# Kernel optimization log

Measured on AMD Instinct MI355X. Metric: run time of the kernel, lower is better.

## Reference

```python
import jax, jax.numpy as jnp
import numpy as np

NHEADS = 16

def setup_inputs() -> dict:
    key = jax.random.key(0)
    ks = jax.random.split(key, 5)
    C = 1024
    d = C // NHEADS
    x  = jax.random.normal(ks[0], (2, 2048, C), dtype=jnp.float32)
    sc = 1.0 / np.sqrt(C)
    wq = jax.random.normal(ks[1], (C, C), dtype=jnp.float32) * sc
    wk = jax.random.normal(ks[2], (C, C), dtype=jnp.float32) * sc
    wv = jax.random.normal(ks[3], (C, C), dtype=jnp.float32) * sc
    wo = jax.random.normal(ks[4], (d, C), dtype=jnp.float32) * (1.0 / np.sqrt(d))
    return {"x": x, "wq": wq, "wk": wk, "wv": wv, "wo": wo}

def reference(x, wq, wk, wv, wo):
    B, T, C = x.shape
    H = NHEADS
    d = C // H

    def split_heads(y):
        return y.reshape(B, T, H, d).transpose(0, 2, 1, 3)  # [B,H,T,d]

    Q = split_heads(x @ wq)
    K = split_heads(x @ wk)
    V = split_heads(x @ wv)

    # scores[b,h,q,k]
    prod = jnp.einsum('bhqd,bhkd->bhqk', Q, K) / np.sqrt(d)

    # ALiBi bias: offset[h, q, k] = (k - q) * 2**(-8*(h+1)/H)
    idx = jnp.arange(T)
    slopes = jnp.exp2(-8.0 * (jnp.arange(H, dtype=jnp.float32) + 1.0) / H)
    bias = (idx[None, :] - idx[:, None]).astype(x.dtype) * slopes[:, None, None]
    prod = prod + bias[None]

    # causal tril mask: keep k <= q
    keep = idx[None, :] <= idx[:, None]  # [T_q, T_k]
    prod = jnp.where(keep[None, None], prod, -jnp.inf)

    # NOTE: original uses F.softmax(prod, 2) -> softmax over the QUERY axis.
    attention_weights = jax.nn.softmax(prod, axis=2)
    attention_output = jnp.einsum('bhqk,bhkd->bhqd', attention_weights, V)

    # per-head wo projection then sum over heads == (sum over heads) @ wo (linear)
    outputs = attention_output.sum(axis=1) @ wo  # [B,T,C]
    return x + outputs
```

## Files before the change

kernel.cpp:

```cpp
#include <hip/hip_runtime.h>
#include <math.h>

#define NB 2
#define NH 16
#define NT 2048
#define ND 64
#define NC 1024
#define L2E 1.44269504f

typedef __attribute__((ext_vector_type(4))) float f32x4;
typedef __attribute__((ext_vector_type(8))) short short8;
typedef __attribute__((ext_vector_type(4))) short short4_t;
typedef __attribute__((ext_vector_type(8))) unsigned short ushort8;
typedef __attribute__((ext_vector_type(4))) unsigned short ushort4_t;

#define GLOAD_LDS(gp, lp)                                                \
    __builtin_amdgcn_global_load_lds(                                    \
        (const __attribute__((address_space(1))) void*)(gp),             \
        (__attribute__((address_space(3))) void*)(lp), 16, 0, 0)

__device__ __forceinline__ int sigma_p(int p) {
    return 4 * ((p >> 3) & 3) + (p & 3) + 16 * ((p >> 2) & 1) + 32 * (p >> 5);
}

__device__ __forceinline__ unsigned short f2bf(float f) {
    unsigned u = __builtin_bit_cast(unsigned, f);
    unsigned r = (u + 0x7FFFu + ((u >> 16) & 1u)) >> 16;
    return (unsigned short)r;
}

__device__ __forceinline__ unsigned cvtpk_bf16(float lo, float hi) {
    unsigned r;
    asm("v_cvt_pk_bf16_f32 %0, %1, %2" : "=v"(r) : "v"(lo), "v"(hi));
    return r;
}

__device__ __forceinline__ f32x4 mfma16(short8 a, short8 b, f32x4 c) {
    return __builtin_amdgcn_mfma_f32_16x16x32_bf16(a, b, c, 0, 0, 0);
}

__device__ __forceinline__ short8 frag_load(const unsigned short* rowp, int g, int half) {
    short8 v;
    short4_t lo = *(const short4_t*)(rowp + 4 * g + 32 * half);
    short4_t hi = *(const short4_t*)(rowp + 4 * g + 16 + 32 * half);
    #pragma unroll
    for (int j = 0; j < 4; ++j) { v[j] = lo[j]; v[4 + j] = hi[j]; }
    return v;
}

__device__ __forceinline__ short8 frag_g(const unsigned short* rowp, int g, int half) {
    return *(const short8*)(rowp + 8 * g + 32 * half);
}

__device__ __forceinline__ short8 frag_swz128(const unsigned short* tile, int row, int g, int half) {
    const char* p = (const char*)tile + row * 128 + (((g + 4 * half) ^ (row & 7)) << 4);
    return *(const short8*)p;
}

__global__ __launch_bounds__(256) void cvt_x(const float* __restrict__ src,
                                             unsigned short* __restrict__ dst, int n4) {
    int i = blockIdx.x * 256 + threadIdx.x;
    if (i >= n4) return;
    const int blk = i >> 4, c4 = i & 15;
    const int gg = (c4 >> 1) & 3, bb = c4 & 1, hh = c4 >> 3;
    f32x4 v = ((const f32x4*)src)[blk * 16 + gg + 4 * bb + 8 * hh];
    ushort4_t o;
    #pragma unroll
    for (int j = 0; j < 4; ++j) o[j] = f2bf(v[j]);
    ((ushort4_t*)dst)[i] = o;
}

__global__ __launch_bounds__(256) void cvtT3(const float* __restrict__ w0,
                                             const float* __restrict__ w1,
                                             const float* __restrict__ w2,
                                             unsigned short* __restrict__ Wt_all) {
    __shared__ __align__(16) float T[64][68];
    const float* W = (blockIdx.z == 0) ? w0 : ((blockIdx.z == 1) ? w1 : w2);
    unsigned short* Wt = Wt_all + (size_t)blockIdx.z * NC * NC;
    const int tid = threadIdx.x;
    const int k0 = blockIdx.x * 64, n0 = blockIdx.y * 64;
    #pragma unroll
    for (int p = 0; p < 4; ++p) {
        int r = 16 * p + (tid >> 4);
        int c = (tid & 15) * 4;
        *(f32x4*)&T[r][c] = *(const f32x4*)&W[(size_t)(k0 + r) * NC + n0 + c];
    }
    __syncthreads();
    const int nr = tid >> 2, kc = (tid & 3) * 16;
    ushort8 o0, o1;
    #pragma unroll
    for (int j = 0; j < 8; ++j) o0[j] = f2bf(T[sigma_p(kc + j)][nr]);
    #pragma unroll
    for (int j = 0; j < 8; ++j) o1[j] = f2bf(T[sigma_p(kc + 8 + j)][nr]);
    unsigned short* q = Wt + (size_t)(n0 + nr) * NC + k0 + kc;
    *(ushort8*)q       = o0;
    *(ushort8*)(q + 8) = o1;
}

__global__ __launch_bounds__(256) void cvtT_wo(const float* __restrict__ W,
                                               unsigned short* __restrict__ Wt) {
    __shared__ __align__(16) float T[64][68];
    const int tid = threadIdx.x;
    const int n0 = blockIdx.y * 64;
    #pragma unroll
    for (int p = 0; p < 4; ++p) {
        int r = 16 * p + (tid >> 4);
        int c = (tid & 15) * 4;
        *(f32x4*)&T[r][c] = *(const f32x4*)&W[(size_t)r * NC + n0 + c];
    }
    __syncthreads();
    const int nr = tid >> 2, kc = (tid & 3) * 16;
    ushort8 o0, o1;
    #pragma unroll
    for (int j = 0; j < 8; ++j) { o0[j] = f2bf(T[kc + j][nr]); o1[j] = f2bf(T[kc + 8 + j][nr]); }
    unsigned short* q = Wt + (size_t)(n0 + nr) * ND + kc;
    *(ushort8*)q       = o0;
    *(ushort8*)(q + 8) = o1;
}

__global__ __launch_bounds__(256) void gemm_qkv(const unsigned short* __restrict__ Xh,
                                                const unsigned short* __restrict__ Wt_all,
                                                unsigned short* __restrict__ qk_dst,
                                                unsigned short* __restrict__ Vt) {
    __shared__ __align__(16) unsigned short Xs[2][8192];
    __shared__ __align__(16) unsigned short Ws[2][8192];
    const int tid = threadIdx.x;
    const int lane = tid & 63, w = tid >> 6;
    const int g = lane >> 4, l15 = lane & 15;
    const int wr = w >> 1, wc = w & 1;
    const int subrow = lane >> 3;
    const int src_off = (((lane & 7) ^ subrow) << 4);
    const int m0 = blockIdx.x * 128;
    const int which = blockIdx.y >> 3;
    const int n0 = (blockIdx.y & 7) * 128;
    const unsigned short* Wt = Wt_all + (size_t)which * NC * NC;

    f32x4 acc[4][4] = {};

    auto stage = [&](int buf, int kk) {
        #pragma unroll
        for (int i = 0; i < 4; ++i) {
            const int r0 = 8 * w + 32 * i;
            const char* xs = (const char*)Xh + (((size_t)(m0 + r0 + subrow) * NC + kk) << 1) + src_off;
            GLOAD_LDS(xs, (char*)&Xs[buf][r0 * 64]);
            const char* ws = (const char*)Wt + (((size_t)(n0 + r0 + subrow) * NC + kk) << 1) + src_off;
            GLOAD_LDS(ws, (char*)&Ws[buf][r0 * 64]);
        }
    };

    stage(0, 0);
    asm volatile("s_waitcnt vmcnt(0)" ::: "memory");
    __builtin_amdgcn_s_barrier();
    int cur = 0;

    for (int kk = 0; kk < NC; kk += 64) {
        if (kk + 64 < NC) stage(cur ^ 1, kk + 64);
        short8 a[4][2], b[4][2];
        #pragma unroll
        for (int mr = 0; mr < 4; ++mr) {
            a[mr][0] = frag_swz128(Xs[cur], 64 * wr + 16 * mr + l15, g, 0);
            a[mr][1] = frag_swz128(Xs[cur], 64 * wr + 16 * mr + l15, g, 1);
        }
        #pragma unroll
        for (int nc = 0; nc < 4; ++nc) {
            b[nc][0] = frag_swz128(Ws[cur], 64 * wc + 16 * nc + l15, g, 0);
            b[nc][1] = frag_swz128(Ws[cur], 64 * wc + 16 * nc + l15, g, 1);
        }
        #pragma unroll
        for (int mr = 0; mr < 4; ++mr)
            #pragma unroll
            for (int nc = 0; nc < 4; ++nc) {
                acc[mr][nc] = mfma16(a[mr][0], b[nc][0], acc[mr][nc]);
                acc[mr][nc] = mfma16(a[mr][1], b[nc][1], acc[mr][nc]);
            }
        asm volatile("s_waitcnt vmcnt(0)" ::: "memory");
        __builtin_amdgcn_s_barrier();
        cur ^= 1;
    }

    if (which < 2) {
        unsigned short* dst = qk_dst + (size_t)which * (NB * NH * NT * ND);
        #pragma unroll
        for (int mr = 0; mr < 4; ++mr) {
            #pragma unroll
            for (int nc = 0; nc < 4; ++nc) {
                const int n = n0 + 64 * wc + 16 * nc + l15;
                const int hh = n >> 6;
                const int dd = 32 * (nc >> 1) + 8 * (l15 >> 2) + 4 * (nc & 1) + (l15 & 3);
                #pragma unroll
                for (int r = 0; r < 4; ++r) {
                    const int m = m0 + 64 * wr + 16 * mr + 4 * g + r;
                    const int bb = m >> 11, tt = m & (NT - 1);
                    dst[(((size_t)bb * NH + hh) * NT + tt) * ND + dd] = f2bf(acc[mr][nc][r]);
                }
            }
        }
    } else {
        #pragma unroll
        for (int mr = 0; mr < 4; ++mr) {
            const int m = m0 + 64 * wr + 16 * mr + 4 * g;
            const int bb = m >> 11, tt = m & (NT - 1);
            const int tbase = (tt & ~63) + 32 * (mr >> 1) + 8 * g + 4 * (mr & 1);
            #pragma unroll
            for (int nc = 0; nc < 4; ++nc) {
                const int n = n0 + 64 * wc + 16 * nc + l15;
                const int hh = n >> 6, dd = n & 63;
                ushort4_t o;
                #pragma unroll
                for (int r = 0; r < 4; ++r) o[r] = f2bf(acc[mr][nc][r]);
                *(ushort4_t*)&Vt[(((size_t)bb * NH + hh) * ND + dd) * NT + tbase] = o;
            }
        }
    }
}

__global__ __launch_bounds__(256, 4) void colstats(const unsigned short* __restrict__ Qh,
                                                   const unsigned short* __restrict__ Kh,
                                                   float* __restrict__ Lc2) {
    __shared__ __align__(16) unsigned short Qs[3][4096];
    const int tid = threadIdx.x;
    const int lane = tid & 63, w = tid >> 6;
    const int g = lane >> 4, l15 = lane & 15;
    const int subrow = lane >> 3;
    const int src_off = (((lane & 7) ^ subrow) << 4);
    const int lin = blockIdx.x + 32 * blockIdx.y;
    const int xcd = lin & 7, idx = lin >> 3;
    const int bh = xcd * 4 + (idx & 3);
    const int rest = idx >> 2;
    const int j = rest >> 1, par = rest & 1;
    const int jA = j, jB = 31 - j;
    const int hh = bh & (NH - 1);
    const float slL2 = exp2f(-0.5f * (float)(hh + 1)) * L2E;
    const float C1 = 0.125f * L2E;
    const float s16 = 16.f * slL2;

    const int K0A = 64 * jA, K0B = 64 * jB;
    const unsigned short* krA = Kh + ((size_t)bh * NT + K0A + 16 * w + l15) * ND;
    const unsigned short* krB = Kh + ((size_t)bh * NT + K0B + 16 * w + l15) * ND;
    const short8 akA0 = frag_g(krA, g, 0), akA1 = frag_g(krA, g, 1);
    const short8 akB0 = frag_g(krB, g, 0), akB1 = frag_g(krB, g, 1);
    const int kA0 = K0A + 16 * w + 4 * g;
    const int kB0 = K0B + 16 * w + 4 * g;

    const char* Qbase = (const char*)(Qh + (size_t)bh * NT * ND);
    auto stage = [&](int buf, int q0) {
        const char* qs = Qbase + (size_t)(q0 + 16 * w + subrow) * 128 + src_off;
        char* qd = (char*)&Qs[buf][16 * w * 64];
        GLOAD_LDS(qs, qd);
        GLOAD_LDS(qs + 1024, qd + 1024);
    };

    f32x4 accA = {}, accB = {};
    float rs[4];
    #pragma unroll
    for (int r = 0; r < 4; ++r) rs[r] = (float)r * slL2;

    const int qt0 = jA + ((par ^ jA) & 1);
    stage(0, 64 * qt0);
    stage(1, 64 * (qt0 + 2));
    int cur = 0, nxt = 2;

    auto strip = [&](const short8* qf, const short8& a0, const short8& a1,
                     f32x4& acc, float b0, bool mask) {
        #pragma unroll
        for (int q4 = 0; q4 < 4; ++q4) {
            f32x4 d = {};
            __builtin_amdgcn_s_setprio(1);
            d = mfma16(a0, qf[2 * q4], d);
            d = mfma16(a1, qf[2 * q4 + 1], d);
            __builtin_amdgcn_s_setprio(0);
            #pragma unroll
            for (int r = 0; r < 4; ++r) {
                float e = exp2f(fmaf(d[r], C1, b0 + rs[r]));
                if (mask && (16 * q4 + l15 < 16 * w + 4 * g + r)) e = 0.f;
                acc[r] += e;
            }
            b0 -= s16;
        }
    };

    for (int qt = qt0; qt < 32; qt += 2) {
        if (qt + 2 < 32) asm volatile("s_waitcnt vmcnt(2)" ::: "memory");
        else             asm volatile("s_waitcnt vmcnt(0)" ::: "memory");
        __builtin_amdgcn_s_barrier();
        if (qt + 4 < 32) stage(nxt, 64 * (qt + 4));
        const unsigned short* tile = Qs[cur];
        short8 qf[8];
        #pragma unroll
        for (int q4 = 0; q4 < 4; ++q4) {
            qf[2 * q4]     = frag_swz128(tile, 16 * q4 + l15, g, 0);
            qf[2 * q4 + 1] = frag_swz128(tile, 16 * q4 + l15, g, 1);
        }
        const int q0 = 64 * qt;
        strip(qf, akA0, akA1, accA, (float)(kA0 - q0 - l15) * slL2, qt == jA);
        if (qt >= jB)
            strip(qf, akB0, akB1, accB, (float)(kB0 - q0 - l15) * slL2, qt == jB);
        cur = (cur == 2) ? 0 : cur + 1;
        nxt = (nxt == 2) ? 0 : nxt + 1;
    }
    #pragma unroll
    for (int off = 1; off <= 8; off <<= 1) {
        #pragma unroll
        for (int r = 0; r < 4; ++r) {
            accA[r] += __shfl_xor(accA[r], off);
            accB[r] += __shfl_xor(accB[r], off);
        }
    }
    if (l15 == 0) {
        float* Lp = Lc2 + (size_t)(par * 32 + bh) * NT;
        #pragma unroll
        for (int r = 0; r < 4; ++r) {
            Lp[kA0 + r] = accA[r];
            Lp[kB0 + r] = accB[r];
        }
    }
}

__global__ __launch_bounds__(256) void attn_pv(const unsigned short* __restrict__ Qh,
                                               const unsigned short* __restrict__ Kh,
                                               const unsigned short* __restrict__ Vt,
                                               const float* __restrict__ Lc2,
                                               float* __restrict__ att) {
    __shared__ __align__(16) unsigned short Ks[3][4096];
    __shared__ __align__(16) unsigned short Vs[3][4096];
    __shared__ __align__(16) float Ls[NT];
    const int tid = threadIdx.x;
    const int lane = tid & 63, w = tid >> 6;
    const int g = lane >> 4, l15 = lane & 15;
    const int subrow = lane >> 3;
    const int src_off = (((lane & 7) ^ subrow) << 4);
    const int lin = blockIdx.x + 16 * blockIdx.y;
    const int xcd = lin & 7, idx = lin >> 3;
    const int bh = xcd * 4 + (idx & 3);
    const int j = idx >> 2;
    const int jA = j, jB = 31 - j;
    const int Q0A = 64 * jA, Q0B = 64 * jB;
    const int qA = Q0A + 16 * w + l15;
    const int qB = Q0B + 16 * w + l15;
    const int hh = bh & (NH - 1);
    const int bb = bh >> 4;
    const float slL2 = exp2f(-0.5f * (float)(hh + 1)) * L2E;
    const float C1 = 0.125f * L2E;

    short8 bqA0, bqA1, bqB0, bqB1;
    {
        const unsigned short* qr = Qh + ((size_t)bh * NT + qA) * ND;
        bqA0 = frag_g(qr, g, 0);
        bqA1 = frag_g(qr, g, 1);
        qr = Qh + ((size_t)bh * NT + qB) * ND;
        bqB0 = frag_g(qr, g, 0);
        bqB1 = frag_g(qr, g, 1);
    }

    auto stageKV = [&](int buf, int K0) {
        const char* ksrc = (const char*)Kh + (size_t)((size_t)bh * NT + K0 + 16 * w + subrow) * 128 + src_off;
        char* kdst = (char*)&Ks[buf][16 * w * 64];
        GLOAD_LDS(ksrc, kdst);
        GLOAD_LDS(ksrc + 1024, kdst + 1024);
        const char* vsrc = (const char*)Vt + ((((size_t)bh * ND + 16 * w + subrow) * NT + K0) << 1) + src_off;
        char* vdst = (char*)&Vs[buf][16 * w * 64];
        GLOAD_LDS(vsrc, vdst);
        GLOAD_LDS(vsrc + 8 * NT * 2, vdst + 1024);
    };

    stageKV(0, 0);
    stageKV(1, 64);
    {
        const f32x4* La = (const f32x4*)(Lc2 + (size_t)bh * NT);
        const f32x4* Lb = (const f32x4*)(Lc2 + (size_t)(32 + bh) * NT);
        const int nv = (jB + 1) * 16;
        for (int i = tid; i < nv; i += 256) {
            f32x4 a = La[i], b = Lb[i];
            float kb = (float)(4 * i);
            f32x4 v;
            #pragma unroll
            for (int c = 0; c < 4; ++c)
                v[c] = log2f(a[c] + b[c]) - (kb + (float)c) * slL2;
            ((f32x4*)Ls)[i] = v;
        }
    }
    asm volatile("s_waitcnt lgkmcnt(0)" ::: "memory");
    int cur = 0, nxt = 2;

    f32x4 oA[4] = {}, oB[4] = {};
    const float qsA = (float)qA * slL2;
    const float qsB = (float)qB * slL2;

    auto dostrip = [&](const short8* kf, const short8* vf,
                       const short8& q0f, const short8& q1f, f32x4 (&o)[4],
                       float qsc, int q, int K0, bool mask) {
        f32x4 pacc[4];
        __builtin_amdgcn_s_setprio(1);
        #pragma unroll
        for (int s4 = 0; s4 < 4; ++s4) {
            f32x4 d = {};
            d = mfma16(kf[2 * s4], q0f, d);
            d = mfma16(kf[2 * s4 + 1], q1f, d);
            pacc[s4] = d;
        }
        __builtin_amdgcn_s_setprio(0);
        union { unsigned u[4]; short8 s; } pa[2];
        #pragma unroll
        for (int s4 = 0; s4 < 4; ++s4) {
            f32x4 Lf = *(const f32x4*)&Ls[K0 + 16 * s4 + 4 * g];
            float p[4];
            #pragma unroll
            for (int r = 0; r < 4; ++r)
                p[r] = exp2f(fmaf(pacc[s4][r], C1, -(Lf[r] + qsc)));
            if (mask) {
                #pragma unroll
                for (int r = 0; r < 4; ++r)
                    if (K0 + 16 * s4 + 4 * g + r > q) p[r] = 0.f;
            }
            pa[s4 >> 1].u[2 * (s4 & 1)]     = cvtpk_bf16(p[0], p[1]);
            pa[s4 >> 1].u[2 * (s4 & 1) + 1] = cvtpk_bf16(p[2], p[3]);
        }
        __builtin_amdgcn_s_setprio(1);
        #pragma unroll
        for (int n = 0; n < 4; ++n) {
            o[n] = mfma16(pa[0].s, vf[2 * n], o[n]);
            o[n] = mfma16(pa[1].s, vf[2 * n + 1], o[n]);
        }
        __builtin_amdgcn_s_setprio(0);
    };

    for (int kt = 0; kt <= jB; ++kt) {
        if (kt < jB) asm volatile("s_waitcnt vmcnt(4)" ::: "memory");
        else         asm volatile("s_waitcnt vmcnt(0)" ::: "memory");
        __builtin_amdgcn_s_barrier();
        if (kt + 2 <= jB) stageKV(nxt, 64 * (kt + 2));
        const int K0 = 64 * kt;
        short8 kf[8], vf[8];
        #pragma unroll
        for (int s4 = 0; s4 < 4; ++s4) {
            kf[2 * s4]     = frag_swz128(Ks[cur], 16 * s4 + l15, g, 0);
            kf[2 * s4 + 1] = frag_swz128(Ks[cur], 16 * s4 + l15, g, 1);
            vf[2 * s4]     = frag_swz128(Vs[cur], 16 * s4 + l15, g, 0);
            vf[2 * s4 + 1] = frag_swz128(Vs[cur], 16 * s4 + l15, g, 1);
        }
        dostrip(kf, vf, bqB0, bqB1, oB, qsB, qB, K0, kt == jB);
        if (kt <= jA)
            dostrip(kf, vf, bqA0, bqA1, oA, qsA, qA, K0, kt == jA);
        cur = (cur == 2) ? 0 : cur + 1;
        nxt = (nxt == 2) ? 0 : nxt + 1;
    }
    #pragma unroll
    for (int n = 0; n < 4; ++n) {
        #pragma unroll
        for (int r = 0; r < 4; ++r) {
            att[(((size_t)bb * NT + Q0A + 16 * w + 4 * g + r) * NH + hh) * ND + 16 * n + l15] = oA[n][r];
            att[(((size_t)bb * NT + Q0B + 16 * w + 4 * g + r) * NH + hh) * ND + 16 * n + l15] = oB[n][r];
        }
    }
}

__global__ __launch_bounds__(256) void headsum(const float* __restrict__ att,
                                               unsigned short* __restrict__ A) {
    const int row = blockIdx.x * 16 + (threadIdx.x >> 4);
    const int d0 = (threadIdx.x & 15) * 4;
    const float* p = att + (size_t)row * (NH * ND) + d0;
    f32x4 s = {};
    #pragma unroll
    for (int h = 0; h < NH; ++h)
        s += *(const f32x4*)(p + h * ND);
    ushort4_t o;
    #pragma unroll
    for (int j = 0; j < 4; ++j) o[j] = f2bf(s[j]);
    *(ushort4_t*)&A[(size_t)row * ND + d0] = o;
}

__global__ __launch_bounds__(256) void out_proj(const float* __restrict__ x,
                                                const unsigned short* __restrict__ A,
                                                const unsigned short* __restrict__ Wot,
                                                float* __restrict__ out) {
    const int tid = threadIdx.x;
    const int lane = tid & 63, w = tid >> 6;
    const int g = lane >> 4, l15 = lane & 15;
    const int m0 = blockIdx.x * 64, n0 = blockIdx.y * 64;

    const unsigned short* ar = A + (size_t)(m0 + 16 * w + l15) * ND;
    short8 a0 = frag_load(ar, g, 0);
    short8 a1 = frag_load(ar, g, 1);

    f32x4 acc[4] = {};
    #pragma unroll
    for (int ns = 0; ns < 4; ++ns) {
        const unsigned short* br = Wot + (size_t)(n0 + 16 * ns + l15) * ND;
        acc[ns] = mfma16(a0, frag_load(br, g, 0), acc[ns]);
        acc[ns] = mfma16(a1, frag_load(br, g, 1), acc[ns]);
    }
    #pragma unroll
    for (int ns = 0; ns < 4; ++ns) {
        #pragma unroll
        for (int r = 0; r < 4; ++r) {
            int m = m0 + 16 * w + 4 * g + r;
            int n = n0 + 16 * ns + l15;
            out[(size_t)m * NC + n] = x[(size_t)m * NC + n] + acc[ns][r];
        }
    }
}

extern "C" void kernel_launch(void* const* d_in, const int* in_sizes, int n_in,
                              void* d_out, int out_size, void* d_ws, size_t ws_size,
                              hipStream_t stream) {
    const float* x  = (const float*)d_in[0];
    const float* wq = (const float*)d_in[1];
    const float* wk = (const float*)d_in[2];
    const float* wv = (const float*)d_in[3];
    const float* wo = (const float*)d_in[4];
    float* out = (float*)d_out;

    const size_t MB = 1u << 20;
    const size_t KB = 1u << 10;
    unsigned char* w8 = (unsigned char*)d_ws;
    unsigned short* Xh  = (unsigned short*)(w8);
    unsigned short* Wta = (unsigned short*)(w8 + 8 * MB);
    unsigned short* Qh  = (unsigned short*)(w8 + 16 * MB);
    unsigned short* Kh  = (unsigned short*)(w8 + 24 * MB);
    unsigned short* Vt  = (unsigned short*)(w8 + 32 * MB);
    float*          att = (float*)(w8 + 40 * MB);
    float*          Lc2 = (float*)(w8 + 56 * MB);
    unsigned short* A   = (unsigned short*)(w8 + 56 * MB + 512 * KB);
    unsigned short* Wot = (unsigned short*)(w8 + 57 * MB);

    cvt_x<<<(NB * NT * NC) / 1024, 256, 0, stream>>>(x, Xh, (NB * NT * NC) / 4);
    cvtT3<<<dim3(16, 16, 3), 256, 0, stream>>>(wq, wk, wv, Wta);
    cvtT_wo<<<dim3(1, 16), 256, 0, stream>>>(wo, Wot);

    gemm_qkv<<<dim3(32, 24), 256, 0, stream>>>(Xh, Wta, Qh, Vt);

    colstats<<<dim3(32, 32), 256, 0, stream>>>(Qh, Kh, Lc2);
    attn_pv<<<dim3(16, 32), 256, 0, stream>>>(Qh, Kh, Vt, Lc2, att);

    headsum<<<(NB * NT) / 16, 256, 0, stream>>>(att, A);
    out_proj<<<dim3(64, 16), 256, 0, stream>>>(x, A, Wot, out);
}
```

Baseline: 142.7 us.

## Split attn_pv query strips across 8 waves instead of 4

The attn_pv kernel now launches 512 threads per block. Waves 0-3 handle the late (B) query strip and waves 4-7 the early (A) strip, where before each wave processed both strips one after the other. K/V staging is spread over 8 waves with one load each, and the vmcnt waits are adjusted to match. This doubles the number of waves that can hide latency and halves each wave's serial work. In exchange, the A-strip waves sit idle after their causal range ends but must still reach every barrier, and the higher thread count per block may limit occupancy through register pressure.

Result: no change. 141.1 us (-1.1%).

```diff
diff --git a/kernel.cpp b/kernel.cpp
--- a/kernel.cpp
+++ b/kernel.cpp
@@ -316,7 +316,7 @@
     }
 }
 
-__global__ __launch_bounds__(256) void attn_pv(const unsigned short* __restrict__ Qh,
+__global__ __launch_bounds__(512) void attn_pv(const unsigned short* __restrict__ Qh,
                                                const unsigned short* __restrict__ Kh,
                                                const unsigned short* __restrict__ Vt,
                                                const float* __restrict__ Lc2,
@@ -334,33 +334,29 @@
     const int bh = xcd * 4 + (idx & 3);
     const int j = idx >> 2;
     const int jA = j, jB = 31 - j;
-    const int Q0A = 64 * jA, Q0B = 64 * jB;
-    const int qA = Q0A + 16 * w + l15;
-    const int qB = Q0B + 16 * w + l15;
     const int hh = bh & (NH - 1);
     const int bb = bh >> 4;
     const float slL2 = exp2f(-0.5f * (float)(hh + 1)) * L2E;
     const float C1 = 0.125f * L2E;
 
-    short8 bqA0, bqA1, bqB0, bqB1;
+    const bool isB = (w < 4);
+    const int wl = isB ? w : (w - 4);
+    const int Q0 = isB ? 64 * jB : 64 * jA;
+    const int myJ = isB ? jB : jA;
+    const int q = Q0 + 16 * wl + l15;
+
+    short8 bq0, bq1;
     {
-        const unsigned short* qr = Qh + ((size_t)bh * NT + qA) * ND;
-        bqA0 = frag_g(qr, g, 0);
-        bqA1 = frag_g(qr, g, 1);
-        qr = Qh + ((size_t)bh * NT + qB) * ND;
-        bqB0 = frag_g(qr, g, 0);
-        bqB1 = frag_g(qr, g, 1);
+        const unsigned short* qr = Qh + ((size_t)bh * NT + q) * ND;
+        bq0 = frag_g(qr, g, 0);
+        bq1 = frag_g(qr, g, 1);
     }
 
     auto stageKV = [&](int buf, int K0) {
-        const char* ksrc = (const char*)Kh + (size_t)((size_t)bh * NT + K0 + 16 * w + subrow) * 128 + src_off;
-        char* kdst = (char*)&Ks[buf][16 * w * 64];
-        GLOAD_LDS(ksrc, kdst);
-        GLOAD_LDS(ksrc + 1024, kdst + 1024);
-        const char* vsrc = (const char*)Vt + ((((size_t)bh * ND + 16 * w + subrow) * NT + K0) << 1) + src_off;
-        char* vdst = (char*)&Vs[buf][16 * w * 64];
-        GLOAD_LDS(vsrc, vdst);
-        GLOAD_LDS(vsrc + 8 * NT * 2, vdst + 1024);
+        const char* ksrc = (const char*)Kh + (size_t)((size_t)bh * NT + K0 + 8 * w + subrow) * 128 + src_off;
+        GLOAD_LDS(ksrc, (char*)&Ks[buf][8 * w * 64]);
+        const char* vsrc = (const char*)Vt + ((((size_t)bh * ND + 8 * w + subrow) * NT + K0) << 1) + src_off;
+        GLOAD_LDS(vsrc, (char*)&Vs[buf][8 * w * 64]);
     };
 
     stageKV(0, 0);
@@ -369,7 +365,7 @@
         const f32x4* La = (const f32x4*)(Lc2 + (size_t)bh * NT);
         const f32x4* Lb = (const f32x4*)(Lc2 + (size_t)(32 + bh) * NT);
         const int nv = (jB + 1) * 16;
-        for (int i = tid; i < nv; i += 256) {
+        for (int i = tid; i < nv; i += 512) {
             f32x4 a = La[i], b = Lb[i];
             float kb = (float)(4 * i);
             f32x4 v;
@@ -382,20 +378,17 @@
     asm volatile("s_waitcnt lgkmcnt(0)" ::: "memory");
     int cur = 0, nxt = 2;
 
-    f32x4 oA[4] = {}, oB[4] = {};
-    const float qsA = (float)qA * slL2;
-    const float qsB = (float)qB * slL2;
-
-    auto dostrip = [&](const short8* kf, const short8* vf,
-                       const short8& q0f, const short8& q1f, f32x4 (&o)[4],
-                       float qsc, int q, int K0, bool mask) {
+    f32x4 o[4] = {};
+    const float qsc = (float)q * slL2;
+
+    auto dostrip = [&](const short8* kf, const short8* vf, int K0, bool mask) {
         f32x4 pacc[4];
         __builtin_amdgcn_s_setprio(1);
         #pragma unroll
         for (int s4 = 0; s4 < 4; ++s4) {
             f32x4 d = {};
-            d = mfma16(kf[2 * s4], q0f, d);
-            d = mfma16(kf[2 * s4 + 1], q1f, d);
+            d = mfma16(kf[2 * s4], bq0, d);
+            d = mfma16(kf[2 * s4 + 1], bq1, d);
             pacc[s4] = d;
         }
         __builtin_amdgcn_s_setprio(0);
@@ -425,22 +418,22 @@
     };
 
     for (int kt = 0; kt <= jB; ++kt) {
-        if (kt < jB) asm volatile("s_waitcnt vmcnt(4)" ::: "memory");
+        if (kt < jB) asm volatile("s_waitcnt vmcnt(2)" ::: "memory");
         else         asm volatile("s_waitcnt vmcnt(0)" ::: "memory");
         __builtin_amdgcn_s_barrier();
         if (kt + 2 <= jB) stageKV(nxt, 64 * (kt + 2));
-        const int K0 = 64 * kt;
-        short8 kf[8], vf[8];
-        #pragma unroll
-        for (int s4 = 0; s4 < 4; ++s4) {
-            kf[2 * s4]     = frag_swz128(Ks[cur], 16 * s4 + l15, g, 0);
-            kf[2 * s4 + 1] = frag_swz128(Ks[cur], 16 * s4 + l15, g, 1);
-            vf[2 * s4]     = frag_swz128(Vs[cur], 16 * s4 + l15, g, 0);
-            vf[2 * s4 + 1] = frag_swz128(Vs[cur], 16 * s4 + l15, g, 1);
-        }
-        dostrip(kf, vf, bqB0, bqB1, oB, qsB, qB, K0, kt == jB);
-        if (kt <= jA)
-            dostrip(kf, vf, bqA0, bqA1, oA, qsA, qA, K0, kt == jA);
+        if (kt <= myJ) {
+            const int K0 = 64 * kt;
+            short8 kf[8], vf[8];
+            #pragma unroll
+            for (int s4 = 0; s4 < 4; ++s4) {
+                kf[2 * s4]     = frag_swz128(Ks[cur], 16 * s4 + l15, g, 0);
+                kf[2 * s4 + 1] = frag_swz128(Ks[cur], 16 * s4 + l15, g, 1);
+                vf[2 * s4]     = frag_swz128(Vs[cur], 16 * s4 + l15, g, 0);
+                vf[2 * s4 + 1] = frag_swz128(Vs[cur], 16 * s4 + l15, g, 1);
+            }
+            dostrip(kf, vf, K0, kt == myJ);
+        }
         cur = (cur == 2) ? 0 : cur + 1;
         nxt = (nxt == 2) ? 0 : nxt + 1;
     }
@@ -448,8 +441,7 @@
     for (int n = 0; n < 4; ++n) {
         #pragma unroll
         for (int r = 0; r < 4; ++r) {
-            att[(((size_t)bb * NT + Q0A + 16 * w + 4 * g + r) * NH + hh) * ND + 16 * n + l15] = oA[n][r];
-            att[(((size_t)bb * NT + Q0B + 16 * w + 4 * g + r) * NH + hh) * ND + 16 * n + l15] = oB[n][r];
+            att[(((size_t)bb * NT + Q0 + 16 * wl + 4 * g + r) * NH + hh) * ND + 16 * n + l15] = o[n][r];
         }
     }
 }
@@ -530,7 +522,7 @@
     gemm_qkv<<<dim3(32, 24), 256, 0, stream>>>(Xh, Wta, Qh, Vt);
 
     colstats<<<dim3(32, 32), 256, 0, stream>>>(Qh, Kh, Lc2);
-    attn_pv<<<dim3(16, 32), 256, 0, stream>>>(Qh, Kh, Vt, Lc2, att);
+    attn_pv<<<dim3(16, 32), 512, 0, stream>>>(Qh, Kh, Vt, Lc2, att);
 
     headsum<<<(NB * NT) / 16, 256, 0, stream>>>(att, A);
     out_proj<<<dim3(64, 16), 256, 0, stream>>>(x, A, Wot, out);
```
